# Kernel tuning notes

Measured on AMD Instinct MI355X. Metric: run time of the kernel, lower is better.

Reference implementation:

```python
import jax, jax.numpy as jnp
import numpy as np

B, T, D, H = 2, 2048, 2048, 32
HD = D // H
# quantization scales (constructor-time attributes in the original repo)
A_PROJ = 3e-4   # q/k/v proj alpha (W8A8B8O8Linear)
A_QK = 2e-5     # qk_bmm alpha (BMM_S8T_S8N_F32T)
A_PV = 1e-2     # pv_bmm alpha (BMM_S8T_S8N_S8T)
A_OUT = 1e-4    # out_proj alpha (W8A8BFP32OFP32Linear)


def _i8(key, shape):
    return jax.random.randint(key, shape, -128, 128, dtype=jnp.int32).astype(jnp.int8)


def setup_inputs() -> dict:
    key = jax.random.key(0)
    ks = jax.random.split(key, 10)
    hidden_states = _i8(ks[0], (B, T, D))
    # causal mask, 0 on/below diagonal, large negative above
    causal = jnp.triu(jnp.full((T, T), -1e9, dtype=jnp.float32), k=1)
    attention_mask = jnp.broadcast_to(causal, (B, 1, T, T))
    return {
        "hidden_states": hidden_states,
        "attention_mask": attention_mask,
        "Wq": _i8(ks[1], (D, D)), "bq": _i8(ks[2], (D,)),
        "Wk": _i8(ks[3], (D, D)), "bk": _i8(ks[4], (D,)),
        "Wv": _i8(ks[5], (D, D)), "bv": _i8(ks[6], (D,)),
        "Wo": _i8(ks[7], (D, D)),
        "bo": jax.random.normal(ks[8], (D,), dtype=jnp.float32),
    }


def _w8a8b8o8(x_i8, W_i8, b_i8, alpha):
    # int8 GEMM -> int32 accum; epilogue: alpha*acc + bias, saturate to int8
    acc = jnp.einsum('btk,nk->btn', x_i8.astype(jnp.int32), W_i8.astype(jnp.int32))
    y = alpha * acc.astype(jnp.float32) + b_i8.astype(jnp.float32)
    return jnp.clip(jnp.round(y), -128, 127).astype(jnp.int8)


def reference(hidden_states, attention_mask, Wq, bq, Wk, bk, Wv, bv, Wo, bo):
    # q/k/v projections: int8 in, int8 out
    q = _w8a8b8o8(hidden_states, Wq, bq, A_PROJ)
    k = _w8a8b8o8(hidden_states, Wk, bk, A_PROJ)
    v = _w8a8b8o8(hidden_states, Wv, bv, A_PROJ)

    def shape(x):  # [B,T,D] -> [B,H,T,HD]
        return x.reshape(B, T, H, HD).transpose(0, 2, 1, 3)

    qh, kh, vh = shape(q), shape(k), shape(v)

    # qk_bmm (BMM_S8T_S8N_F32T): fp32 = alpha * int8 q @ k^T
    attn = A_QK * jnp.einsum('bhtd,bhsd->bhts',
                             qh.astype(jnp.int32), kh.astype(jnp.int32)).astype(jnp.float32)
    attn = attn + attention_mask  # [B,1,T,T] broadcasts over heads
    attn = jnp.maximum(attn, jnp.finfo(jnp.float32).min)
    probs = jax.nn.softmax(attn, axis=-1)

    # quantize probs: p.mul_(127).round_() -> int8
    p_i8 = jnp.clip(jnp.round(probs * 127.0), -128, 127).astype(jnp.int8)

    # pv_bmm (BMM_S8T_S8N_S8T): int8 out = sat(round(alpha * p @ v))
    pv = jnp.einsum('bhts,bhsd->bhtd', p_i8.astype(jnp.int32), vh.astype(jnp.int32))
    attn_out_i8 = jnp.clip(jnp.round(A_PV * pv.astype(jnp.float32)), -128, 127).astype(jnp.int8)

    # [B,H,T,HD] -> [B,T,D]
    attn_out = attn_out_i8.transpose(0, 2, 1, 3).reshape(B, T, D)

    # out_proj (W8A8BFP32OFP32Linear): fp32 = alpha*(x@W^T) + fp32 bias
    acc = jnp.einsum('btk,nk->btn', attn_out.astype(jnp.int32), Wo.astype(jnp.int32))
    out = A_OUT * acc.astype(jnp.float32) + bo
    return out
```

## Files before the change

### kernel.cpp

```cpp
#include <hip/hip_runtime.h>
#include <cstdint>

#define A_PROJ 3e-4f
#define A_QK   2e-5f
#define A_PV   1e-2f
#define A_OUT  1e-4f

#define NB 2
#define NT 2048
#define ND 2048
#define NH 32
#define NHD 64
#define NM (NB*NT)

typedef int v4i __attribute__((ext_vector_type(4)));

__device__ __forceinline__ int8_t sat8(float y) {
  float r = rintf(y);
  r = fminf(fmaxf(r, -128.f), 127.f);
  return (int8_t)(int)r;
}

__device__ __forceinline__ void gl2lds16(const int8_t* g, int8_t* l) {
  __builtin_amdgcn_global_load_lds(
      (const __attribute__((address_space(1))) void*)g,
      (__attribute__((address_space(3))) void*)l, 16, 0, 0);
}

__global__ void pack_i8(const int* __restrict__ src, int8_t* __restrict__ dst, int n4) {
  int i = blockIdx.x * blockDim.x + threadIdx.x;
  if (i >= n4) return;
  int4 v = ((const int4*)src)[i];
  uint32_t p = (uint32_t)(v.x & 255) | ((uint32_t)(v.y & 255) << 8) |
               ((uint32_t)(v.z & 255) << 16) | ((uint32_t)(v.w & 255) << 24);
  ((uint32_t*)dst)[i] = p;
}

__global__ __launch_bounds__(256) void gemm_qkv(
    const int8_t* __restrict__ X,
    const int8_t* __restrict__ Wq, const int8_t* __restrict__ Wk, const int8_t* __restrict__ Wv,
    const int* __restrict__ bq, const int* __restrict__ bk, const int* __restrict__ bv,
    int8_t* __restrict__ Qh, int8_t* __restrict__ Kh, int8_t* __restrict__ Vt)
{
  __shared__ __align__(16) int8_t As[2][128][64];
  __shared__ __align__(16) int8_t Bs[2][128][64];
  const int z = blockIdx.z;
  const int8_t* W  = (z == 0) ? Wq : ((z == 1) ? Wk : Wv);
  const int* bias  = (z == 0) ? bq : ((z == 1) ? bk : bv);
  const int m0 = blockIdx.x * 128, n0 = blockIdx.y * 128;
  const int tid = threadIdx.x, lane = tid & 63, wave = tid >> 6;
  const int wm = wave >> 1, wn = wave & 1;
  const int l15 = lane & 15, quad = lane >> 4;

  const int srow = lane >> 2;
  const int scol = (lane & 3) * 16;

  v4i acc[4][4];
  const v4i vzero = {0, 0, 0, 0};
  #pragma unroll
  for (int i = 0; i < 4; ++i)
    #pragma unroll
    for (int j = 0; j < 4; ++j) acc[i][j] = vzero;

  for (int k0 = 0; k0 < ND; k0 += 128) {
    #pragma unroll
    for (int j = 0; j < 8; ++j) {
      int slot = j * 4 + wave;
      int sl = slot & 15;
      int h = sl >> 3, rblk = sl & 7;
      int row = rblk * 16 + srow;
      if (slot < 16) {
        gl2lds16(&X[(size_t)(m0 + row) * ND + k0 + h * 64 + scol], &As[h][rblk * 16][0]);
      } else {
        gl2lds16(&W[(size_t)(n0 + row) * ND + k0 + h * 64 + scol], &Bs[h][rblk * 16][0]);
      }
    }
    __syncthreads();
    #pragma unroll
    for (int h = 0; h < 2; ++h) {
      v4i a[4], b[4];
      #pragma unroll
      for (int mt = 0; mt < 4; ++mt) a[mt] = *(const v4i*)&As[h][wm*64 + mt*16 + l15][quad*16];
      #pragma unroll
      for (int nt = 0; nt < 4; ++nt) b[nt] = *(const v4i*)&Bs[h][wn*64 + nt*16 + l15][quad*16];
      #pragma unroll
      for (int mt = 0; mt < 4; ++mt)
        #pragma unroll
        for (int nt = 0; nt < 4; ++nt)
          acc[mt][nt] = __builtin_amdgcn_mfma_i32_16x16x64_i8(a[mt], b[nt], acc[mt][nt], 0, 0, 0);
    }
    __syncthreads();
  }

  float bf[4];
  #pragma unroll
  for (int nt = 0; nt < 4; ++nt) bf[nt] = (float)bias[n0 + wn*64 + nt*16 + l15];

  #pragma unroll
  for (int mt = 0; mt < 4; ++mt)
    #pragma unroll
    for (int nt = 0; nt < 4; ++nt)
      #pragma unroll
      for (int r = 0; r < 4; ++r) {
        int m = m0 + wm*64 + mt*16 + quad*4 + r;
        int n = n0 + wn*64 + nt*16 + l15;
        int8_t q = sat8(A_PROJ * (float)acc[mt][nt][r] + bf[nt]);
        int bb = m >> 11, t = m & (NT - 1);
        int h = n >> 6, hd = n & (NHD - 1);
        size_t bh = (size_t)bb * NH + h;
        if (z == 2) Vt[(bh * NHD + hd) * NT + t] = q;
        else ((z == 0) ? Qh : Kh)[(bh * NT + t) * NHD + hd] = q;
      }
}

__global__ __launch_bounds__(256) void attn_fused(
    const int8_t* __restrict__ Qh, const int8_t* __restrict__ Kh, const int8_t* __restrict__ Vt,
    int8_t* __restrict__ AO)
{
  __shared__ __align__(16) int8_t Qs[128][80];
  __shared__ __align__(16) int8_t Ks[128][80];
  __shared__ __align__(16) int8_t Vs[64][144];
  __shared__ __align__(16) uint32_t Ps32[4][32][36];

  const int bh = blockIdx.y;
  const int tid = threadIdx.x, lane = tid & 63, wave = tid >> 6;
  const int l15 = lane & 15, quad = lane >> 4;
  const v4i vzero = {0, 0, 0, 0};
  const float MAGIC = 12582912.0f;

  const int8_t* Qp = Qh + (size_t)bh * NT * NHD;
  const int8_t* Kp = Kh + (size_t)bh * NT * NHD;
  const int8_t* Vp = Vt + (size_t)bh * NHD * NT;
  const int bb = bh >> 5, h = bh & (NH - 1);

  for (int half = 0; half < 2; ++half) {
    const int xq = half ? (15 - (int)blockIdx.x) : (int)blockIdx.x;
    const int t0 = xq * 128;

    __syncthreads();
    #pragma unroll
    for (int it = 0; it < 2; ++it) {
      int c = tid + it * 256;
      int row = c >> 2, c16 = (c & 3) * 16;
      *(int4*)&Qs[row][c16] = *(const int4*)&Qp[(size_t)(t0 + row) * NHD + c16];
    }
    __syncthreads();
    v4i qf[2];
    #pragma unroll
    for (int nt = 0; nt < 2; ++nt) qf[nt] = *(const v4i*)&Qs[wave*32 + nt*16 + l15][quad*16];
    const int tme0 = t0 + wave * 32 + l15;

    float lsum[2] = {0.f, 0.f};
    for (int st = 0; st < xq; ++st) {
      const int s0 = st * 128;
      #pragma unroll
      for (int it = 0; it < 2; ++it) {
        int c = tid + it * 256;
        int row = c >> 2, c16 = (c & 3) * 16;
        *(int4*)&Ks[row][c16] = *(const int4*)&Kp[(size_t)(s0 + row) * NHD + c16];
      }
      __syncthreads();
      v4i kf[8];
      #pragma unroll
      for (int mt = 0; mt < 8; ++mt) kf[mt] = *(const v4i*)&Ks[mt*16 + l15][quad*16];
      #pragma unroll
      for (int nt = 0; nt < 2; ++nt) {
        float acc = 0.f;
        #pragma unroll
        for (int mt = 0; mt < 8; ++mt) {
          v4i sa = __builtin_amdgcn_mfma_i32_16x16x64_i8(kf[mt], qf[nt], vzero, 0, 0, 0);
          #pragma unroll
          for (int r = 0; r < 4; ++r) acc += __expf(A_QK * (float)sa[r]);
        }
        lsum[nt] += acc;
      }
      __syncthreads();
    }
    {
      const int s0 = xq * 128;
      #pragma unroll
      for (int it = 0; it < 2; ++it) {
        int c = tid + it * 256;
        int row = c >> 2, c16 = (c & 3) * 16;
        *(int4*)&Ks[row][c16] = *(const int4*)&Kp[(size_t)(s0 + row) * NHD + c16];
      }
      __syncthreads();
      v4i kf[8];
      #pragma unroll
      for (int mt = 0; mt < 8; ++mt) kf[mt] = *(const v4i*)&Ks[mt*16 + l15][quad*16];
      #pragma unroll
      for (int nt = 0; nt < 2; ++nt) {
        const int t = tme0 + nt * 16;
        float acc = 0.f;
        #pragma unroll
        for (int mt = 0; mt < 8; ++mt) {
          v4i sa = __builtin_amdgcn_mfma_i32_16x16x64_i8(kf[mt], qf[nt], vzero, 0, 0, 0);
          const int sbase = s0 + mt*16 + quad*4;
          #pragma unroll
          for (int r = 0; r < 4; ++r) {
            float e = __expf(A_QK * (float)sa[r]);
            acc += (sbase + r <= t) ? e : 0.f;
          }
        }
        lsum[nt] += acc;
      }
      __syncthreads();
    }
    float linv[2];
    #pragma unroll
    for (int nt = 0; nt < 2; ++nt) {
      float v = lsum[nt];
      v += __shfl_xor(v, 16, 64);
      v += __shfl_xor(v, 32, 64);
      linv[nt] = 127.0f / v;
    }

    v4i accv[2][4];
    #pragma unroll
    for (int i = 0; i < 2; ++i)
      #pragma unroll
      for (int j = 0; j < 4; ++j) accv[i][j] = vzero;

    for (int st = 0; st <= xq; ++st) {
      const int s0 = st * 128;
      const bool diag = (st == xq);
      #pragma unroll
      for (int it = 0; it < 2; ++it) {
        int c = tid + it * 256;
        int row = c >> 2, c16 = (c & 3) * 16;
        *(int4*)&Ks[row][c16] = *(const int4*)&Kp[(size_t)(s0 + row) * NHD + c16];
      }
      #pragma unroll
      for (int it = 0; it < 2; ++it) {
        int c = tid + it * 256;
        int row = c >> 3, c16 = (c & 7) * 16;
        *(int4*)&Vs[row][c16] = *(const int4*)&Vp[(size_t)row * NT + s0 + c16];
      }
      __syncthreads();
      v4i kf[8];
      #pragma unroll
      for (int mt = 0; mt < 8; ++mt) kf[mt] = *(const v4i*)&Ks[mt*16 + l15][quad*16];

      if (!diag) {
        #pragma unroll
        for (int nt = 0; nt < 2; ++nt) {
          #pragma unroll
          for (int mt = 0; mt < 8; ++mt) {
            v4i sa = __builtin_amdgcn_mfma_i32_16x16x64_i8(kf[mt], qf[nt], vzero, 0, 0, 0);
            uint32_t pk = 0;
            #pragma unroll
            for (int r = 0; r < 4; ++r) {
              float e = __expf(A_QK * (float)sa[r]);
              float f = fmaf(e, linv[nt], MAGIC);
              pk |= (__float_as_uint(f) & 0xFFu) << (8 * r);
            }
            Ps32[wave][nt*16 + l15][mt*4 + quad] = pk;
          }
        }
      } else {
        #pragma unroll
        for (int nt = 0; nt < 2; ++nt) {
          const int t = tme0 + nt * 16;
          #pragma unroll
          for (int mt = 0; mt < 8; ++mt) {
            v4i sa = __builtin_amdgcn_mfma_i32_16x16x64_i8(kf[mt], qf[nt], vzero, 0, 0, 0);
            uint32_t pk = 0;
            const int sbase = s0 + mt*16 + quad*4;
            #pragma unroll
            for (int r = 0; r < 4; ++r) {
              float e = (sbase + r <= t) ? __expf(A_QK * (float)sa[r]) : 0.f;
              float f = fmaf(e, linv[nt], MAGIC);
              pk |= (__float_as_uint(f) & 0xFFu) << (8 * r);
            }
            Ps32[wave][nt*16 + l15][mt*4 + quad] = pk;
          }
        }
      }
      #pragma unroll
      for (int ks = 0; ks < 2; ++ks) {
        v4i ap[2], bv[4];
        #pragma unroll
        for (int mt2 = 0; mt2 < 2; ++mt2)
          ap[mt2] = *(const v4i*)&Ps32[wave][mt2*16 + l15][ks*16 + quad*4];
        #pragma unroll
        for (int nt2 = 0; nt2 < 4; ++nt2)
          bv[nt2] = *(const v4i*)&Vs[nt2*16 + l15][ks*64 + quad*16];
        #pragma unroll
        for (int mt2 = 0; mt2 < 2; ++mt2)
          #pragma unroll
          for (int nt2 = 0; nt2 < 4; ++nt2)
            accv[mt2][nt2] = __builtin_amdgcn_mfma_i32_16x16x64_i8(ap[mt2], bv[nt2], accv[mt2][nt2], 0, 0, 0);
      }
      __syncthreads();
    }

    #pragma unroll
    for (int mt2 = 0; mt2 < 2; ++mt2)
      #pragma unroll
      for (int nt2 = 0; nt2 < 4; ++nt2)
        #pragma unroll
        for (int r = 0; r < 4; ++r) {
          int t = t0 + wave*32 + mt2*16 + quad*4 + r;
          int d = nt2*16 + l15;
          AO[((size_t)bb * NT + t) * ND + h * NHD + d] = sat8(A_PV * (float)accv[mt2][nt2][r]);
        }
  }
}

__global__ __launch_bounds__(256) void gemm_out(
    const int8_t* __restrict__ X, const int8_t* __restrict__ W,
    const float* __restrict__ bo, float* __restrict__ out)
{
  __shared__ __align__(16) int8_t As[2][128][64];
  __shared__ __align__(16) int8_t Bs[2][128][64];
  const int m0 = blockIdx.x * 128, n0 = blockIdx.y * 128;
  const int tid = threadIdx.x, lane = tid & 63, wave = tid >> 6;
  const int wm = wave >> 1, wn = wave & 1;
  const int l15 = lane & 15, quad = lane >> 4;
  const int srow = lane >> 2, scol = (lane & 3) * 16;

  v4i acc[4][4];
  const v4i vzero = {0, 0, 0, 0};
  #pragma unroll
  for (int i = 0; i < 4; ++i)
    #pragma unroll
    for (int j = 0; j < 4; ++j) acc[i][j] = vzero;

  for (int k0 = 0; k0 < ND; k0 += 128) {
    #pragma unroll
    for (int j = 0; j < 8; ++j) {
      int slot = j * 4 + wave;
      int sl = slot & 15;
      int h = sl >> 3, rblk = sl & 7;
      int row = rblk * 16 + srow;
      if (slot < 16) {
        gl2lds16(&X[(size_t)(m0 + row) * ND + k0 + h * 64 + scol], &As[h][rblk * 16][0]);
      } else {
        gl2lds16(&W[(size_t)(n0 + row) * ND + k0 + h * 64 + scol], &Bs[h][rblk * 16][0]);
      }
    }
    __syncthreads();
    #pragma unroll
    for (int h = 0; h < 2; ++h) {
      v4i a[4], b[4];
      #pragma unroll
      for (int mt = 0; mt < 4; ++mt) a[mt] = *(const v4i*)&As[h][wm*64 + mt*16 + l15][quad*16];
      #pragma unroll
      for (int nt = 0; nt < 4; ++nt) b[nt] = *(const v4i*)&Bs[h][wn*64 + nt*16 + l15][quad*16];
      #pragma unroll
      for (int mt = 0; mt < 4; ++mt)
        #pragma unroll
        for (int nt = 0; nt < 4; ++nt)
          acc[mt][nt] = __builtin_amdgcn_mfma_i32_16x16x64_i8(a[mt], b[nt], acc[mt][nt], 0, 0, 0);
    }
    __syncthreads();
  }

  float bf[4];
  #pragma unroll
  for (int nt = 0; nt < 4; ++nt) bf[nt] = bo[n0 + wn*64 + nt*16 + l15];

  #pragma unroll
  for (int mt = 0; mt < 4; ++mt)
    #pragma unroll
    for (int nt = 0; nt < 4; ++nt)
      #pragma unroll
      for (int r = 0; r < 4; ++r) {
        int m = m0 + wm*64 + mt*16 + quad*4 + r;
        int n = n0 + wn*64 + nt*16 + l15;
        out[(size_t)m * ND + n] = A_OUT * (float)acc[mt][nt][r] + bf[nt];
      }
}

extern "C" void kernel_launch(void* const* d_in, const int* in_sizes, int n_in,
                              void* d_out, int out_size, void* d_ws, size_t ws_size,
                              hipStream_t stream)
{
  const int*   hs  = (const int*)d_in[0];
  const int*   Wq  = (const int*)d_in[2];
  const int*   bq  = (const int*)d_in[3];
  const int*   Wk  = (const int*)d_in[4];
  const int*   bkb = (const int*)d_in[5];
  const int*   Wv  = (const int*)d_in[6];
  const int*   bvb = (const int*)d_in[7];
  const int*   Wo  = (const int*)d_in[8];
  const float* bo  = (const float*)d_in[9];
  float* out = (float*)d_out;

  char* ws = (char*)d_ws;
  const size_t SZ_X = (size_t)NM * ND;
  const size_t SZ_W = (size_t)ND * ND;
  const size_t SZ_H = (size_t)NB * NH * NT * NHD;
  int8_t* Xp  = (int8_t*)ws;
  int8_t* Wqp = (int8_t*)(ws + SZ_X);
  int8_t* Wkp = Wqp + SZ_W;
  int8_t* Wvp = Wkp + SZ_W;
  int8_t* Wop = Wvp + SZ_W;
  int8_t* Qh  = Wop + SZ_W;
  int8_t* Kh  = Qh + SZ_H;
  int8_t* Vt  = Kh + SZ_H;
  int8_t* AO  = Xp;

  pack_i8<<<(int)((SZ_X/4 + 255) / 256), 256, 0, stream>>>(hs, Xp, (int)(SZ_X/4));
  pack_i8<<<(int)((SZ_W/4 + 255) / 256), 256, 0, stream>>>(Wq, Wqp, (int)(SZ_W/4));
  pack_i8<<<(int)((SZ_W/4 + 255) / 256), 256, 0, stream>>>(Wk, Wkp, (int)(SZ_W/4));
  pack_i8<<<(int)((SZ_W/4 + 255) / 256), 256, 0, stream>>>(Wv, Wvp, (int)(SZ_W/4));
  pack_i8<<<(int)((SZ_W/4 + 255) / 256), 256, 0, stream>>>(Wo, Wop, (int)(SZ_W/4));

  gemm_qkv<<<dim3(NM/128, ND/128, 3), 256, 0, stream>>>(Xp, Wqp, Wkp, Wvp, bq, bkb, bvb, Qh, Kh, Vt);
  attn_fused<<<dim3(8, NB*NH), 256, 0, stream>>>(Qh, Kh, Vt, AO);
  gemm_out<<<dim3(NM/128, ND/128), 256, 0, stream>>>(AO, Wop, bo, out);
}
```

Before: 363.5 us.

## Retile attention to 64-row query blocks, swizzle LDS, fuse pack kernels

Merges the five int8 pack launches into one kernel. Adds an XOR swizzle to the LDS tiles of both GEMMs and the attention kernel to cut bank conflicts. Restructures attention so each block handles 64 query rows per half, with one 16-row tile per wave, which doubles the grid. It also switches K/V staging to direct global-to-LDS loads and uses hardware exp2 with a folded log2e constant. The smaller query tiles mean K/V tiles are reloaded more often relative to compute, and exp2 may round slightly differently from the previous exp, which could flip int8 rounding of probabilities.

```diff
diff --git a/kernel.cpp b/kernel.cpp
--- a/kernel.cpp
+++ b/kernel.cpp
@@ -21,19 +21,38 @@
   return (int8_t)(int)r;
 }
 
+__device__ __forceinline__ float exp2_fast(float x) {
+  return __builtin_amdgcn_exp2f(x);
+}
+
 __device__ __forceinline__ void gl2lds16(const int8_t* g, int8_t* l) {
   __builtin_amdgcn_global_load_lds(
       (const __attribute__((address_space(1))) void*)g,
       (__attribute__((address_space(3))) void*)l, 16, 0, 0);
 }
 
-__global__ void pack_i8(const int* __restrict__ src, int8_t* __restrict__ dst, int n4) {
+#define NWW (ND*ND/4)
+__global__ void pack_all(const int* __restrict__ X,
+                         const int* __restrict__ W0, const int* __restrict__ W1,
+                         const int* __restrict__ W2, const int* __restrict__ W3,
+                         int8_t* __restrict__ dX, int8_t* __restrict__ dW0,
+                         int8_t* __restrict__ dW1, int8_t* __restrict__ dW2,
+                         int8_t* __restrict__ dW3) {
   int i = blockIdx.x * blockDim.x + threadIdx.x;
-  if (i >= n4) return;
-  int4 v = ((const int4*)src)[i];
+  const int nx = NM*ND/4;
+  const int* src; int8_t* dst; int off;
+  if (i < nx) { src = X; dst = dX; off = i; }
+  else {
+    int j = i - nx;
+    int r = j >> 20;
+    off = j & (NWW - 1);
+    src = (r == 0) ? W0 : (r == 1) ? W1 : (r == 2) ? W2 : W3;
+    dst = (r == 0) ? dW0 : (r == 1) ? dW1 : (r == 2) ? dW2 : dW3;
+  }
+  int4 v = ((const int4*)src)[off];
   uint32_t p = (uint32_t)(v.x & 255) | ((uint32_t)(v.y & 255) << 8) |
                ((uint32_t)(v.z & 255) << 16) | ((uint32_t)(v.w & 255) << 24);
-  ((uint32_t*)dst)[i] = p;
+  ((uint32_t*)dst)[off] = p;
 }
 
 __global__ __launch_bounds__(256) void gemm_qkv(
@@ -53,7 +72,8 @@
   const int l15 = lane & 15, quad = lane >> 4;
 
   const int srow = lane >> 2;
-  const int scol = (lane & 3) * 16;
+  const int scol = (((lane & 3) ^ ((lane >> 3) & 3)) * 16);
+  const int rqcol = (quad ^ ((l15 >> 1) & 3)) * 16;
 
   v4i acc[4][4];
   const v4i vzero = {0, 0, 0, 0};
@@ -67,22 +87,22 @@
     for (int j = 0; j < 8; ++j) {
       int slot = j * 4 + wave;
       int sl = slot & 15;
-      int h = sl >> 3, rblk = sl & 7;
+      int hh = sl >> 3, rblk = sl & 7;
       int row = rblk * 16 + srow;
       if (slot < 16) {
-        gl2lds16(&X[(size_t)(m0 + row) * ND + k0 + h * 64 + scol], &As[h][rblk * 16][0]);
+        gl2lds16(&X[(size_t)(m0 + row) * ND + k0 + hh * 64 + scol], &As[hh][rblk * 16][0]);
       } else {
-        gl2lds16(&W[(size_t)(n0 + row) * ND + k0 + h * 64 + scol], &Bs[h][rblk * 16][0]);
+        gl2lds16(&W[(size_t)(n0 + row) * ND + k0 + hh * 64 + scol], &Bs[hh][rblk * 16][0]);
       }
     }
     __syncthreads();
     #pragma unroll
-    for (int h = 0; h < 2; ++h) {
+    for (int hh = 0; hh < 2; ++hh) {
       v4i a[4], b[4];
       #pragma unroll
-      for (int mt = 0; mt < 4; ++mt) a[mt] = *(const v4i*)&As[h][wm*64 + mt*16 + l15][quad*16];
-      #pragma unroll
-      for (int nt = 0; nt < 4; ++nt) b[nt] = *(const v4i*)&Bs[h][wn*64 + nt*16 + l15][quad*16];
+      for (int mt = 0; mt < 4; ++mt) a[mt] = *(const v4i*)&As[hh][wm*64 + mt*16 + l15][rqcol];
+      #pragma unroll
+      for (int nt = 0; nt < 4; ++nt) b[nt] = *(const v4i*)&Bs[hh][wn*64 + nt*16 + l15][rqcol];
       #pragma unroll
       for (int mt = 0; mt < 4; ++mt)
         #pragma unroll
@@ -106,8 +126,8 @@
         int n = n0 + wn*64 + nt*16 + l15;
         int8_t q = sat8(A_PROJ * (float)acc[mt][nt][r] + bf[nt]);
         int bb = m >> 11, t = m & (NT - 1);
-        int h = n >> 6, hd = n & (NHD - 1);
-        size_t bh = (size_t)bb * NH + h;
+        int hd8 = n >> 6, hd = n & (NHD - 1);
+        size_t bh = (size_t)bb * NH + hd8;
         if (z == 2) Vt[(bh * NHD + hd) * NT + t] = q;
         else ((z == 0) ? Qh : Kh)[(bh * NT + t) * NHD + hd] = q;
       }
@@ -117,193 +137,142 @@
     const int8_t* __restrict__ Qh, const int8_t* __restrict__ Kh, const int8_t* __restrict__ Vt,
     int8_t* __restrict__ AO)
 {
-  __shared__ __align__(16) int8_t Qs[128][80];
-  __shared__ __align__(16) int8_t Ks[128][80];
-  __shared__ __align__(16) int8_t Vs[64][144];
-  __shared__ __align__(16) uint32_t Ps32[4][32][36];
-
+  __shared__ __align__(16) int8_t Ks[128][64];
+  __shared__ __align__(16) int8_t Vs[64][128];
+  __shared__ __align__(16) uint32_t Ps32[4][16][36];
+
+  const int bx = blockIdx.x;
   const int bh = blockIdx.y;
   const int tid = threadIdx.x, lane = tid & 63, wave = tid >> 6;
   const int l15 = lane & 15, quad = lane >> 4;
   const v4i vzero = {0, 0, 0, 0};
   const float MAGIC = 12582912.0f;
+  const float C2 = 2.8853900817779268e-05f;
 
   const int8_t* Qp = Qh + (size_t)bh * NT * NHD;
   const int8_t* Kp = Kh + (size_t)bh * NT * NHD;
   const int8_t* Vp = Vt + (size_t)bh * NHD * NT;
-  const int bb = bh >> 5, h = bh & (NH - 1);
+  const int bb = bh >> 5, hhead = bh & (NH - 1);
+
+  const int kst_row = lane >> 2;
+  const int kst_col = (((lane & 3) ^ ((lane >> 3) & 3)) * 16);
+  const int vst_row = lane >> 3;
+  const int vst_col = (((lane & 7) ^ ((lane >> 3) & 7)) * 16);
+  const int kfcol = (quad ^ ((l15 >> 1) & 3)) * 16;
 
   for (int half = 0; half < 2; ++half) {
-    const int xq = half ? (15 - (int)blockIdx.x) : (int)blockIdx.x;
-    const int t0 = xq * 128;
-
-    __syncthreads();
-    #pragma unroll
-    for (int it = 0; it < 2; ++it) {
-      int c = tid + it * 256;
-      int row = c >> 2, c16 = (c & 3) * 16;
-      *(int4*)&Qs[row][c16] = *(const int4*)&Qp[(size_t)(t0 + row) * NHD + c16];
-    }
-    __syncthreads();
-    v4i qf[2];
-    #pragma unroll
-    for (int nt = 0; nt < 2; ++nt) qf[nt] = *(const v4i*)&Qs[wave*32 + nt*16 + l15][quad*16];
-    const int tme0 = t0 + wave * 32 + l15;
-
-    float lsum[2] = {0.f, 0.f};
-    for (int st = 0; st < xq; ++st) {
+    const int xq = half ? (31 - bx) : bx;
+    const int t0 = xq * 64;
+    const int sd = xq >> 1;
+    const int tme = t0 + wave * 16 + l15;
+
+    v4i qf = *(const v4i*)&Qp[(size_t)(t0 + wave * 16 + l15) * NHD + quad * 16];
+
+    float lsum = 0.f;
+    for (int st = 0; st <= sd; ++st) {
       const int s0 = st * 128;
       #pragma unroll
-      for (int it = 0; it < 2; ++it) {
-        int c = tid + it * 256;
-        int row = c >> 2, c16 = (c & 3) * 16;
-        *(int4*)&Ks[row][c16] = *(const int4*)&Kp[(size_t)(s0 + row) * NHD + c16];
-      }
+      for (int j = 0; j < 2; ++j)
+        gl2lds16(&Kp[(size_t)(s0 + j*64 + wave*16 + kst_row) * NHD + kst_col],
+                 &Ks[j*64 + wave*16][0]);
       __syncthreads();
       v4i kf[8];
       #pragma unroll
-      for (int mt = 0; mt < 8; ++mt) kf[mt] = *(const v4i*)&Ks[mt*16 + l15][quad*16];
-      #pragma unroll
-      for (int nt = 0; nt < 2; ++nt) {
-        float acc = 0.f;
+      for (int mt = 0; mt < 8; ++mt) kf[mt] = *(const v4i*)&Ks[mt*16 + l15][kfcol];
+      if (st < sd) {
         #pragma unroll
         for (int mt = 0; mt < 8; ++mt) {
-          v4i sa = __builtin_amdgcn_mfma_i32_16x16x64_i8(kf[mt], qf[nt], vzero, 0, 0, 0);
+          v4i sa = __builtin_amdgcn_mfma_i32_16x16x64_i8(kf[mt], qf, vzero, 0, 0, 0);
           #pragma unroll
-          for (int r = 0; r < 4; ++r) acc += __expf(A_QK * (float)sa[r]);
-        }
-        lsum[nt] += acc;
-      }
-      __syncthreads();
-    }
-    {
-      const int s0 = xq * 128;
-      #pragma unroll
-      for (int it = 0; it < 2; ++it) {
-        int c = tid + it * 256;
-        int row = c >> 2, c16 = (c & 3) * 16;
-        *(int4*)&Ks[row][c16] = *(const int4*)&Kp[(size_t)(s0 + row) * NHD + c16];
-      }
-      __syncthreads();
-      v4i kf[8];
-      #pragma unroll
-      for (int mt = 0; mt < 8; ++mt) kf[mt] = *(const v4i*)&Ks[mt*16 + l15][quad*16];
-      #pragma unroll
-      for (int nt = 0; nt < 2; ++nt) {
-        const int t = tme0 + nt * 16;
-        float acc = 0.f;
+          for (int r = 0; r < 4; ++r) lsum += exp2_fast(C2 * (float)sa[r]);
+        }
+      } else {
         #pragma unroll
         for (int mt = 0; mt < 8; ++mt) {
-          v4i sa = __builtin_amdgcn_mfma_i32_16x16x64_i8(kf[mt], qf[nt], vzero, 0, 0, 0);
+          v4i sa = __builtin_amdgcn_mfma_i32_16x16x64_i8(kf[mt], qf, vzero, 0, 0, 0);
           const int sbase = s0 + mt*16 + quad*4;
           #pragma unroll
           for (int r = 0; r < 4; ++r) {
-            float e = __expf(A_QK * (float)sa[r]);
-            acc += (sbase + r <= t) ? e : 0.f;
+            float e = exp2_fast(C2 * (float)sa[r]);
+            lsum += (sbase + r <= tme) ? e : 0.f;
           }
         }
-        lsum[nt] += acc;
       }
       __syncthreads();
     }
-    float linv[2];
-    #pragma unroll
-    for (int nt = 0; nt < 2; ++nt) {
-      float v = lsum[nt];
-      v += __shfl_xor(v, 16, 64);
-      v += __shfl_xor(v, 32, 64);
-      linv[nt] = 127.0f / v;
-    }
-
-    v4i accv[2][4];
-    #pragma unroll
-    for (int i = 0; i < 2; ++i)
-      #pragma unroll
-      for (int j = 0; j < 4; ++j) accv[i][j] = vzero;
-
-    for (int st = 0; st <= xq; ++st) {
+    {
+      lsum += __shfl_xor(lsum, 16, 64);
+      lsum += __shfl_xor(lsum, 32, 64);
+    }
+    const float linv = 127.0f / lsum;
+
+    v4i accv[4];
+    #pragma unroll
+    for (int j = 0; j < 4; ++j) accv[j] = vzero;
+
+    for (int st = 0; st <= sd; ++st) {
       const int s0 = st * 128;
-      const bool diag = (st == xq);
-      #pragma unroll
-      for (int it = 0; it < 2; ++it) {
-        int c = tid + it * 256;
-        int row = c >> 2, c16 = (c & 3) * 16;
-        *(int4*)&Ks[row][c16] = *(const int4*)&Kp[(size_t)(s0 + row) * NHD + c16];
-      }
-      #pragma unroll
-      for (int it = 0; it < 2; ++it) {
-        int c = tid + it * 256;
-        int row = c >> 3, c16 = (c & 7) * 16;
-        *(int4*)&Vs[row][c16] = *(const int4*)&Vp[(size_t)row * NT + s0 + c16];
-      }
+      #pragma unroll
+      for (int j = 0; j < 2; ++j)
+        gl2lds16(&Kp[(size_t)(s0 + j*64 + wave*16 + kst_row) * NHD + kst_col],
+                 &Ks[j*64 + wave*16][0]);
+      #pragma unroll
+      for (int j = 0; j < 2; ++j)
+        gl2lds16(&Vp[(size_t)(j*32 + wave*8 + vst_row) * NT + s0 + vst_col],
+                 &Vs[j*32 + wave*8][0]);
       __syncthreads();
       v4i kf[8];
       #pragma unroll
-      for (int mt = 0; mt < 8; ++mt) kf[mt] = *(const v4i*)&Ks[mt*16 + l15][quad*16];
-
-      if (!diag) {
-        #pragma unroll
-        for (int nt = 0; nt < 2; ++nt) {
+      for (int mt = 0; mt < 8; ++mt) kf[mt] = *(const v4i*)&Ks[mt*16 + l15][kfcol];
+
+      if (st < sd) {
+        #pragma unroll
+        for (int mt = 0; mt < 8; ++mt) {
+          v4i sa = __builtin_amdgcn_mfma_i32_16x16x64_i8(kf[mt], qf, vzero, 0, 0, 0);
+          uint32_t pk = 0;
           #pragma unroll
-          for (int mt = 0; mt < 8; ++mt) {
-            v4i sa = __builtin_amdgcn_mfma_i32_16x16x64_i8(kf[mt], qf[nt], vzero, 0, 0, 0);
-            uint32_t pk = 0;
-            #pragma unroll
-            for (int r = 0; r < 4; ++r) {
-              float e = __expf(A_QK * (float)sa[r]);
-              float f = fmaf(e, linv[nt], MAGIC);
-              pk |= (__float_as_uint(f) & 0xFFu) << (8 * r);
-            }
-            Ps32[wave][nt*16 + l15][mt*4 + quad] = pk;
+          for (int r = 0; r < 4; ++r) {
+            float e = exp2_fast(C2 * (float)sa[r]);
+            float f = fmaf(e, linv, MAGIC);
+            pk |= (__float_as_uint(f) & 0xFFu) << (8 * r);
           }
+          Ps32[wave][l15][mt*4 + quad] = pk;
         }
       } else {
         #pragma unroll
-        for (int nt = 0; nt < 2; ++nt) {
-          const int t = tme0 + nt * 16;
+        for (int mt = 0; mt < 8; ++mt) {
+          v4i sa = __builtin_amdgcn_mfma_i32_16x16x64_i8(kf[mt], qf, vzero, 0, 0, 0);
+          uint32_t pk = 0;
+          const int sbase = s0 + mt*16 + quad*4;
           #pragma unroll
-          for (int mt = 0; mt < 8; ++mt) {
-            v4i sa = __builtin_amdgcn_mfma_i32_16x16x64_i8(kf[mt], qf[nt], vzero, 0, 0, 0);
-            uint32_t pk = 0;
-            const int sbase = s0 + mt*16 + quad*4;
-            #pragma unroll
-            for (int r = 0; r < 4; ++r) {
-              float e = (sbase + r <= t) ? __expf(A_QK * (float)sa[r]) : 0.f;
-              float f = fmaf(e, linv[nt], MAGIC);
-              pk |= (__float_as_uint(f) & 0xFFu) << (8 * r);
-            }
-            Ps32[wave][nt*16 + l15][mt*4 + quad] = pk;
+          for (int r = 0; r < 4; ++r) {
+            float e = (sbase + r <= tme) ? exp2_fast(C2 * (float)sa[r]) : 0.f;
+            float f = fmaf(e, linv, MAGIC);
+            pk |= (__float_as_uint(f) & 0xFFu) << (8 * r);
           }
+          Ps32[wave][l15][mt*4 + quad] = pk;
         }
       }
       #pragma unroll
       for (int ks = 0; ks < 2; ++ks) {
-        v4i ap[2], bv[4];
-        #pragma unroll
-        for (int mt2 = 0; mt2 < 2; ++mt2)
-          ap[mt2] = *(const v4i*)&Ps32[wave][mt2*16 + l15][ks*16 + quad*4];
-        #pragma unroll
-        for (int nt2 = 0; nt2 < 4; ++nt2)
-          bv[nt2] = *(const v4i*)&Vs[nt2*16 + l15][ks*64 + quad*16];
-        #pragma unroll
-        for (int mt2 = 0; mt2 < 2; ++mt2)
-          #pragma unroll
-          for (int nt2 = 0; nt2 < 4; ++nt2)
-            accv[mt2][nt2] = __builtin_amdgcn_mfma_i32_16x16x64_i8(ap[mt2], bv[nt2], accv[mt2][nt2], 0, 0, 0);
+        v4i ap = *(const v4i*)&Ps32[wave][l15][ks*16 + quad*4];
+        #pragma unroll
+        for (int nt2 = 0; nt2 < 4; ++nt2) {
+          v4i bv = *(const v4i*)&Vs[nt2*16 + l15][(((ks*4 + quad) ^ (l15 & 7)) * 16)];
+          accv[nt2] = __builtin_amdgcn_mfma_i32_16x16x64_i8(ap, bv, accv[nt2], 0, 0, 0);
+        }
       }
       __syncthreads();
     }
 
     #pragma unroll
-    for (int mt2 = 0; mt2 < 2; ++mt2)
-      #pragma unroll
-      for (int nt2 = 0; nt2 < 4; ++nt2)
-        #pragma unroll
-        for (int r = 0; r < 4; ++r) {
-          int t = t0 + wave*32 + mt2*16 + quad*4 + r;
-          int d = nt2*16 + l15;
-          AO[((size_t)bb * NT + t) * ND + h * NHD + d] = sat8(A_PV * (float)accv[mt2][nt2][r]);
-        }
+    for (int nt2 = 0; nt2 < 4; ++nt2)
+      #pragma unroll
+      for (int r = 0; r < 4; ++r) {
+        int t = t0 + wave*16 + quad*4 + r;
+        int d = nt2*16 + l15;
+        AO[((size_t)bb * NT + t) * ND + hhead * NHD + d] = sat8(A_PV * (float)accv[nt2][r]);
+      }
   }
 }
 
@@ -317,7 +286,9 @@
   const int tid = threadIdx.x, lane = tid & 63, wave = tid >> 6;
   const int wm = wave >> 1, wn = wave & 1;
   const int l15 = lane & 15, quad = lane >> 4;
-  const int srow = lane >> 2, scol = (lane & 3) * 16;
+  const int srow = lane >> 2;
+  const int scol = (((lane & 3) ^ ((lane >> 3) & 3)) * 16);
+  const int rqcol = (quad ^ ((l15 >> 1) & 3)) * 16;
 
   v4i acc[4][4];
   const v4i vzero = {0, 0, 0, 0};
@@ -331,22 +302,22 @@
     for (int j = 0; j < 8; ++j) {
       int slot = j * 4 + wave;
       int sl = slot & 15;
-      int h = sl >> 3, rblk = sl & 7;
+      int hh = sl >> 3, rblk = sl & 7;
       int row = rblk * 16 + srow;
       if (slot < 16) {
-        gl2lds16(&X[(size_t)(m0 + row) * ND + k0 + h * 64 + scol], &As[h][rblk * 16][0]);
+        gl2lds16(&X[(size_t)(m0 + row) * ND + k0 + hh * 64 + scol], &As[hh][rblk * 16][0]);
       } else {
-        gl2lds16(&W[(size_t)(n0 + row) * ND + k0 + h * 64 + scol], &Bs[h][rblk * 16][0]);
+        gl2lds16(&W[(size_t)(n0 + row) * ND + k0 + hh * 64 + scol], &Bs[hh][rblk * 16][0]);
       }
     }
     __syncthreads();
     #pragma unroll
-    for (int h = 0; h < 2; ++h) {
+    for (int hh = 0; hh < 2; ++hh) {
       v4i a[4], b[4];
       #pragma unroll
-      for (int mt = 0; mt < 4; ++mt) a[mt] = *(const v4i*)&As[h][wm*64 + mt*16 + l15][quad*16];
-      #pragma unroll
-      for (int nt = 0; nt < 4; ++nt) b[nt] = *(const v4i*)&Bs[h][wn*64 + nt*16 + l15][quad*16];
+      for (int mt = 0; mt < 4; ++mt) a[mt] = *(const v4i*)&As[hh][wm*64 + mt*16 + l15][rqcol];
+      #pragma unroll
+      for (int nt = 0; nt < 4; ++nt) b[nt] = *(const v4i*)&Bs[hh][wn*64 + nt*16 + l15][rqcol];
       #pragma unroll
       for (int mt = 0; mt < 4; ++mt)
         #pragma unroll
@@ -401,13 +372,11 @@
   int8_t* Vt  = Kh + SZ_H;
   int8_t* AO  = Xp;
 
-  pack_i8<<<(int)((SZ_X/4 + 255) / 256), 256, 0, stream>>>(hs, Xp, (int)(SZ_X/4));
-  pack_i8<<<(int)((SZ_W/4 + 255) / 256), 256, 0, stream>>>(Wq, Wqp, (int)(SZ_W/4));
-  pack_i8<<<(int)((SZ_W/4 + 255) / 256), 256, 0, stream>>>(Wk, Wkp, (int)(SZ_W/4));
-  pack_i8<<<(int)((SZ_W/4 + 255) / 256), 256, 0, stream>>>(Wv, Wvp, (int)(SZ_W/4));
-  pack_i8<<<(int)((SZ_W/4 + 255) / 256), 256, 0, stream>>>(Wo, Wop, (int)(SZ_W/4));
+  const int ntot = (int)(SZ_X/4 + 4 * (SZ_W/4));
+  pack_all<<<(ntot + 255) / 256, 256, 0, stream>>>(hs, Wq, Wk, Wv, Wo,
+                                                   Xp, Wqp, Wkp, Wvp, Wop);
 
   gemm_qkv<<<dim3(NM/128, ND/128, 3), 256, 0, stream>>>(Xp, Wqp, Wkp, Wvp, bq, bkb, bvb, Qh, Kh, Vt);
-  attn_fused<<<dim3(8, NB*NH), 256, 0, stream>>>(Qh, Kh, Vt, AO);
+  attn_fused<<<dim3(16, NB*NH), 256, 0, stream>>>(Qh, Kh, Vt, AO);
   gemm_out<<<dim3(NM/128, ND/128), 256, 0, stream>>>(AO, Wop, bo, out);
 }
```

Result: faster. 336.2 us (-7.5%).
